# Optimization experiments

Hardware: AMD Instinct MI355X
Metric: run time of the kernel (lower is better)

## Reference

```python
import jax, jax.numpy as jnp
import numpy as np


def _lstm(x, w_ih, w_hh, b_ih, b_hh):
    """Single-layer LSTM over x: [T, in_dim], PyTorch gate order (i, f, g, o).
    Returns (all hidden states [T, H], final hidden [H])."""
    H = w_hh.shape[1]
    # Precompute input contributions for all timesteps in one GEMM: [T, 4H]
    xg = x @ w_ih.T + b_ih + b_hh

    def step(carry, xg_t):
        h, c = carry
        g = xg_t + h @ w_hh.T  # [4H]
        i = jax.nn.sigmoid(g[:H])
        f = jax.nn.sigmoid(g[H:2 * H])
        gg = jnp.tanh(g[2 * H:3 * H])
        o = jax.nn.sigmoid(g[3 * H:])
        c = f * c + i * gg
        h = o * jnp.tanh(c)
        return (h, c), h

    init = (jnp.zeros((H,), x.dtype), jnp.zeros((H,), x.dtype))
    (h_n, _), hs = jax.lax.scan(step, init, xg)
    return hs, h_n


def setup_inputs() -> dict:
    key = jax.random.key(0)
    ks = jax.random.split(key, 9)
    T, F, E = 8192, 256, 512
    Hd = 2 * E  # hidden_dim of rnn1 = 1024
    s = 0.05
    return {
        "x": jax.random.normal(ks[0], (T, F), jnp.float32),
        "w_ih1": jax.random.normal(ks[1], (4 * Hd, F), jnp.float32) * s,
        "w_hh1": jax.random.normal(ks[2], (4 * Hd, Hd), jnp.float32) * s,
        "b_ih1": jax.random.normal(ks[3], (4 * Hd,), jnp.float32) * s,
        "b_hh1": jax.random.normal(ks[4], (4 * Hd,), jnp.float32) * s,
        "w_ih2": jax.random.normal(ks[5], (4 * E, Hd), jnp.float32) * s,
        "w_hh2": jax.random.normal(ks[6], (4 * E, E), jnp.float32) * s,
        "b_ih2": jax.random.normal(ks[7], (4 * E,), jnp.float32) * s,
        "b_hh2": jax.random.normal(ks[8], (4 * E,), jnp.float32) * s,
    }


def reference(x, w_ih1, w_hh1, b_ih1, b_hh1, w_ih2, w_hh2, b_ih2, b_hh2):
    # x reshaped to (1, seq_len, n_features) in torch; batch=1 so work on [T, F].
    hs1, _ = _lstm(x, w_ih1, w_hh1, b_ih1, b_hh1)        # [T, hidden_dim]
    _, h_n = _lstm(hs1, w_ih2, w_hh2, b_ih2, b_hh2)      # [encoding_dim]
    return h_n.reshape((1, -1))                          # (1, encoding_dim)
```

## Files before the change

### kernel.cpp

```cpp
#include <hip/hip_runtime.h>
#include <cstdint>

#define TSTEPS 8192
#define FIN 256
#define HD 1024
#define ED 512
#define W1 128
#define W2 64

#define AG __HIP_MEMORY_SCOPE_AGENT
typedef unsigned long long u64;
typedef unsigned int u32;
typedef u32 u32x4 __attribute__((ext_vector_type(4)));
typedef u32 u32x2 __attribute__((ext_vector_type(2)));

#define DONE1_OFS 12288
#define DONE2_OFS 12416
#define CONS2_OFS 12480

__global__ void init_ctrs(u32* ws32) {
  int i = threadIdx.x;
  if (i < 256) ws32[DONE1_OFS + i] = 0xFFFFFFFFu;
}

__device__ __forceinline__ float sigf(float z) { return 1.0f / (1.0f + expf(-z)); }
__device__ __forceinline__ float uaf(u32 v) { return __uint_as_float(v); }

#define BULK16(pb, want, OK, q0,q1,q2,q3,q4,q5,q6,q7)                          \
  asm volatile(                                                                \
    "global_load_dwordx4 %0, %8, off sc0 sc1\n\t"                              \
    "global_load_dwordx4 %1, %8, off offset:16 sc0 sc1\n\t"                    \
    "global_load_dwordx4 %2, %8, off offset:32 sc0 sc1\n\t"                    \
    "global_load_dwordx4 %3, %8, off offset:48 sc0 sc1\n\t"                    \
    "global_load_dwordx4 %4, %8, off offset:64 sc0 sc1\n\t"                    \
    "global_load_dwordx4 %5, %8, off offset:80 sc0 sc1\n\t"                    \
    "global_load_dwordx4 %6, %8, off offset:96 sc0 sc1\n\t"                    \
    "global_load_dwordx4 %7, %8, off offset:112 sc0 sc1\n\t"                   \
    "s_waitcnt vmcnt(0)"                                                       \
    : "=&v"(q0), "=&v"(q1), "=&v"(q2), "=&v"(q3),                              \
      "=&v"(q4), "=&v"(q5), "=&v"(q6), "=&v"(q7)                               \
    : "v"(pb) : "memory");                                                     \
  OK = (q0.x==want)&(q0.z==want)&(q1.x==want)&(q1.z==want)                     \
     & (q2.x==want)&(q2.z==want)&(q3.x==want)&(q3.z==want)                     \
     & (q4.x==want)&(q4.z==want)&(q5.x==want)&(q5.z==want)                     \
     & (q6.x==want)&(q6.z==want)&(q7.x==want)&(q7.z==want);

__global__ void __launch_bounds__(256, 1) lstm2_fused(
    const float* __restrict__ x,
    const float* __restrict__ w_ih1, const float* __restrict__ w_hh1,
    const float* __restrict__ b_ih1, const float* __restrict__ b_hh1,
    const float* __restrict__ w_ih2, const float* __restrict__ w_hh2,
    const float* __restrict__ b_ih2, const float* __restrict__ b_hh2,
    float* __restrict__ out, u32* __restrict__ ws32)
{
  u64* pair1 = (u64*)ws32;
  u64* pair2 = pair1 + 4 * HD;
  u32* done1 = ws32 + DONE1_OFS;
  u32* done2 = ws32 + DONE2_OFS;
  u32* cons2 = ws32 + CONS2_OFS;

  const int bid  = blockIdx.x;
  const int tid  = threadIdx.x;
  const int wave = tid >> 6;
  const int lane = tid & 63;
  const int half = lane & 1;
  const int kc   = lane >> 1;

  __shared__ float4 hsl[256];
  __shared__ float4 h2l[128];

  if (bid < W1) {
    const int ro = bid * 8 + wave * 2 + half;
    const int kbase  = kc * 32;
    const int xkbase = kc * 8;
    float whh[4][32], wih[4][8], bz[4];
#pragma unroll
    for (int g = 0; g < 4; ++g) {
      const float* wr = w_hh1 + ((size_t)(g * HD + ro)) * HD + kbase;
#pragma unroll
      for (int j = 0; j < 8; ++j) {
        float4 v = *(const float4*)(wr + j * 4);
        whh[g][j*4+0] = v.x; whh[g][j*4+1] = v.y; whh[g][j*4+2] = v.z; whh[g][j*4+3] = v.w;
      }
      const float* ur = w_ih1 + ((size_t)(g * HD + ro)) * FIN + xkbase;
      float4 a = *(const float4*)(ur), b = *(const float4*)(ur + 4);
      wih[g][0]=a.x; wih[g][1]=a.y; wih[g][2]=a.z; wih[g][3]=a.w;
      wih[g][4]=b.x; wih[g][5]=b.y; wih[g][6]=b.z; wih[g][7]=b.w;
      bz[g] = b_ih1[g * HD + ro] + b_hh1[g * HD + ro];
    }
    float cst = 0.f;

    for (int t = 0; t < TSTEPS; ++t) {
      const float* xp = x + (size_t)t * FIN + xkbase;
      float4 xa = *(const float4*)(xp);
      float4 xb = *(const float4*)(xp + 4);

      if (t == 0) {
        hsl[tid] = make_float4(0.f, 0.f, 0.f, 0.f);
      } else if (wave == 0) {
        const u32* d1p = done1 + lane * 2;
        const u32* c2p = cons2 + lane;
        const int wd = t - 1, wc = t - 4;
        u32x2 dv; u32 cv;
        for (;;) {
          asm volatile(
            "global_load_dwordx2 %0, %2, off sc0 sc1\n\t"
            "global_load_dword %1, %3, off sc0 sc1\n\t"
            "s_waitcnt vmcnt(0)"
            : "=&v"(dv), "=&v"(cv) : "v"(d1p), "v"(c2p) : "memory");
          bool ok = ((int)dv.x >= wd) & ((int)dv.y >= wd) & ((int)cv >= wc);
          if (__all(ok)) break;
        }
        const u64* pb = pair1 + (size_t)((t - 1) & 3) * HD + lane * 16;
        const u32 want = (u32)(t - 1);
        u32x4 q0,q1,q2,q3,q4,q5,q6,q7; bool ok;
        for (;;) { BULK16(pb, want, ok, q0,q1,q2,q3,q4,q5,q6,q7); if (__all(ok)) break; }
        const int f0 = lane * 4;
        hsl[(f0+0) ^ (((f0+0)>>3)&7)] = make_float4(uaf(q0.y),uaf(q0.w),uaf(q1.y),uaf(q1.w));
        hsl[(f0+1) ^ (((f0+1)>>3)&7)] = make_float4(uaf(q2.y),uaf(q2.w),uaf(q3.y),uaf(q3.w));
        hsl[(f0+2) ^ (((f0+2)>>3)&7)] = make_float4(uaf(q4.y),uaf(q4.w),uaf(q5.y),uaf(q5.w));
        hsl[(f0+3) ^ (((f0+3)>>3)&7)] = make_float4(uaf(q6.y),uaf(q6.w),uaf(q7.y),uaf(q7.w));
      }
      __syncthreads();

      float hv[32];
#pragma unroll
      for (int j = 0; j < 8; ++j) {
        int f = kc * 8 + j;
        float4 v = hsl[f ^ ((f>>3)&7)];
        hv[j*4+0]=v.x; hv[j*4+1]=v.y; hv[j*4+2]=v.z; hv[j*4+3]=v.w;
      }

      float a0=0.f, a1=0.f, a2=0.f, a3=0.f;
#pragma unroll
      for (int j = 0; j < 32; ++j) {
        float hj = hv[j];
        a0 = fmaf(whh[0][j], hj, a0); a1 = fmaf(whh[1][j], hj, a1);
        a2 = fmaf(whh[2][j], hj, a2); a3 = fmaf(whh[3][j], hj, a3);
      }
      float xvv[8] = {xa.x,xa.y,xa.z,xa.w,xb.x,xb.y,xb.z,xb.w};
#pragma unroll
      for (int j = 0; j < 8; ++j) {
        float xj = xvv[j];
        a0 = fmaf(wih[0][j], xj, a0); a1 = fmaf(wih[1][j], xj, a1);
        a2 = fmaf(wih[2][j], xj, a2); a3 = fmaf(wih[3][j], xj, a3);
      }
#pragma unroll
      for (int d = 2; d < 64; d <<= 1) {
        a0 += __shfl_xor(a0, d, 64);
        a1 += __shfl_xor(a1, d, 64);
        a2 += __shfl_xor(a2, d, 64);
        a3 += __shfl_xor(a3, d, 64);
      }
      float ig = sigf(a0 + bz[0]);
      float fg = sigf(a1 + bz[1]);
      float gg = tanhf(a2 + bz[2]);
      float og = sigf(a3 + bz[3]);
      cst = fg * cst + ig * gg;
      float h = og * tanhf(cst);

      if (lane < 2) {
        u64 pk = ((u64)__float_as_uint(h) << 32) | (u64)(u32)t;
        __hip_atomic_store(pair1 + (size_t)(t & 3) * HD + ro, pk, __ATOMIC_RELAXED, AG);
      }
      __builtin_amdgcn_s_barrier();
      if (tid == 0)
        __hip_atomic_store(done1 + bid, (u32)t, __ATOMIC_RELAXED, AG);
    }
  } else {
    const int jwg = bid - W1;
    const int eo = jwg * 8 + wave * 2 + half;
    const int kbase  = kc * 32;
    const int k2base = kc * 16;
    float wA[4][32], wB[4][16], bz[4];
#pragma unroll
    for (int g = 0; g < 4; ++g) {
      const float* wr = w_ih2 + ((size_t)(g * ED + eo)) * HD + kbase;
#pragma unroll
      for (int j = 0; j < 8; ++j) {
        float4 v = *(const float4*)(wr + j * 4);
        wA[g][j*4+0]=v.x; wA[g][j*4+1]=v.y; wA[g][j*4+2]=v.z; wA[g][j*4+3]=v.w;
      }
      const float* wr2 = w_hh2 + ((size_t)(g * ED + eo)) * ED + k2base;
#pragma unroll
      for (int j = 0; j < 4; ++j) {
        float4 v = *(const float4*)(wr2 + j * 4);
        wB[g][j*4+0]=v.x; wB[g][j*4+1]=v.y; wB[g][j*4+2]=v.z; wB[g][j*4+3]=v.w;
      }
      bz[g] = b_ih2[g * ED + eo] + b_hh2[g * ED + eo];
    }
    float cst = 0.f;

    for (int s = 0; s < TSTEPS; ++s) {
      if (wave == 0) {
        const u32* d1p = done1 + lane * 2;
        u32x2 dv;
        for (;;) {
          asm volatile(
            "global_load_dwordx2 %0, %1, off sc0 sc1\n\t"
            "s_waitcnt vmcnt(0)"
            : "=&v"(dv) : "v"(d1p) : "memory");
          bool ok = ((int)dv.x >= s) & ((int)dv.y >= s);
          if (__all(ok)) break;
        }
        const u64* pb = pair1 + (size_t)(s & 3) * HD + lane * 16;
        const u32 want = (u32)s;
        u32x4 q0,q1,q2,q3,q4,q5,q6,q7; bool ok;
        for (;;) { BULK16(pb, want, ok, q0,q1,q2,q3,q4,q5,q6,q7); if (__all(ok)) break; }
        if (lane == 0)
          __hip_atomic_store(cons2 + jwg, (u32)s, __ATOMIC_RELAXED, AG);
        const int f0 = lane * 4;
        hsl[(f0+0) ^ (((f0+0)>>3)&7)] = make_float4(uaf(q0.y),uaf(q0.w),uaf(q1.y),uaf(q1.w));
        hsl[(f0+1) ^ (((f0+1)>>3)&7)] = make_float4(uaf(q2.y),uaf(q2.w),uaf(q3.y),uaf(q3.w));
        hsl[(f0+2) ^ (((f0+2)>>3)&7)] = make_float4(uaf(q4.y),uaf(q4.w),uaf(q5.y),uaf(q5.w));
        hsl[(f0+3) ^ (((f0+3)>>3)&7)] = make_float4(uaf(q6.y),uaf(q6.w),uaf(q7.y),uaf(q7.w));
      } else if (wave == 1 && s >= 1) {
        const u32* d2p = done2 + lane;
        const int wd = s - 1;
        u32 dv;
        for (;;) {
          asm volatile(
            "global_load_dword %0, %1, off sc0 sc1\n\t"
            "s_waitcnt vmcnt(0)"
            : "=&v"(dv) : "v"(d2p) : "memory");
          if (__all((int)dv >= wd)) break;
        }
        const u64* pb2 = pair2 + (size_t)((s - 1) & 3) * ED + lane * 8;
        const u32 want = (u32)(s - 1);
        u32x4 q0,q1,q2,q3; bool ok;
        for (;;) {
          asm volatile(
            "global_load_dwordx4 %0, %4, off sc0 sc1\n\t"
            "global_load_dwordx4 %1, %4, off offset:16 sc0 sc1\n\t"
            "global_load_dwordx4 %2, %4, off offset:32 sc0 sc1\n\t"
            "global_load_dwordx4 %3, %4, off offset:48 sc0 sc1\n\t"
            "s_waitcnt vmcnt(0)"
            : "=&v"(q0), "=&v"(q1), "=&v"(q2), "=&v"(q3)
            : "v"(pb2) : "memory");
          ok = (q0.x==want)&(q0.z==want)&(q1.x==want)&(q1.z==want)
             & (q2.x==want)&(q2.z==want)&(q3.x==want)&(q3.z==want);
          if (__all(ok)) break;
        }
        const int f0 = lane * 2;
        h2l[(f0+0) ^ (((f0+0)>>3)&7)] = make_float4(uaf(q0.y),uaf(q0.w),uaf(q1.y),uaf(q1.w));
        h2l[(f0+1) ^ (((f0+1)>>3)&7)] = make_float4(uaf(q2.y),uaf(q2.w),uaf(q3.y),uaf(q3.w));
      }
      if (s == 0 && tid < 128) h2l[tid] = make_float4(0.f, 0.f, 0.f, 0.f);
      __syncthreads();

      float hv[32];
#pragma unroll
      for (int j = 0; j < 8; ++j) {
        int f = kc * 8 + j;
        float4 v = hsl[f ^ ((f>>3)&7)];
        hv[j*4+0]=v.x; hv[j*4+1]=v.y; hv[j*4+2]=v.z; hv[j*4+3]=v.w;
      }
      float gv[16];
#pragma unroll
      for (int j = 0; j < 4; ++j) {
        int f = kc * 4 + j;
        float4 v = h2l[f ^ ((f>>3)&7)];
        gv[j*4+0]=v.x; gv[j*4+1]=v.y; gv[j*4+2]=v.z; gv[j*4+3]=v.w;
      }

      float a0=0.f, a1=0.f, a2=0.f, a3=0.f;
#pragma unroll
      for (int j = 0; j < 32; ++j) {
        float hj = hv[j];
        a0 = fmaf(wA[0][j], hj, a0); a1 = fmaf(wA[1][j], hj, a1);
        a2 = fmaf(wA[2][j], hj, a2); a3 = fmaf(wA[3][j], hj, a3);
      }
#pragma unroll
      for (int j = 0; j < 16; ++j) {
        float gj = gv[j];
        a0 = fmaf(wB[0][j], gj, a0); a1 = fmaf(wB[1][j], gj, a1);
        a2 = fmaf(wB[2][j], gj, a2); a3 = fmaf(wB[3][j], gj, a3);
      }
#pragma unroll
      for (int d = 2; d < 64; d <<= 1) {
        a0 += __shfl_xor(a0, d, 64);
        a1 += __shfl_xor(a1, d, 64);
        a2 += __shfl_xor(a2, d, 64);
        a3 += __shfl_xor(a3, d, 64);
      }
      float ig = sigf(a0 + bz[0]);
      float fg = sigf(a1 + bz[1]);
      float gg = tanhf(a2 + bz[2]);
      float og = sigf(a3 + bz[3]);
      cst = fg * cst + ig * gg;
      float h = og * tanhf(cst);

      if (lane < 2) {
        u64 pk = ((u64)__float_as_uint(h) << 32) | (u64)(u32)s;
        __hip_atomic_store(pair2 + (size_t)(s & 3) * ED + eo, pk, __ATOMIC_RELAXED, AG);
        if (s == TSTEPS - 1) out[eo] = h;
      }
      __builtin_amdgcn_s_barrier();
      if (tid == 0)
        __hip_atomic_store(done2 + jwg, (u32)s, __ATOMIC_RELAXED, AG);
    }
  }
}

extern "C" void kernel_launch(void* const* d_in, const int* in_sizes, int n_in,
                              void* d_out, int out_size, void* d_ws, size_t ws_size,
                              hipStream_t stream) {
  const float* x    = (const float*)d_in[0];
  const float* wih1 = (const float*)d_in[1];
  const float* whh1 = (const float*)d_in[2];
  const float* bih1 = (const float*)d_in[3];
  const float* bhh1 = (const float*)d_in[4];
  const float* wih2 = (const float*)d_in[5];
  const float* whh2 = (const float*)d_in[6];
  const float* bih2 = (const float*)d_in[7];
  const float* bhh2 = (const float*)d_in[8];
  float* out = (float*)d_out;
  u32* ws    = (u32*)d_ws;

  hipLaunchKernelGGL(init_ctrs, dim3(1), dim3(256), 0, stream, ws);
  hipLaunchKernelGGL(lstm2_fused, dim3(W1 + W2), dim3(256), 0, stream,
                     x, wih1, whh1, bih1, bhh1, wih2, whh2, bih2, bhh2, out, ws);
}
```

Measured before the change: 36.21 ms.

## Add per-XCC relay blocks that mirror hidden states into XCC-local buffers

Adds extra relay workgroups. One per XCC claims the role via CAS, then polls the global hidden-state ring and copies each step into an XCC-local copy. Compute blocks then poll that local copy with sc0-only loads instead of system-coherent ones, so the cross-XCC coherence traffic of the polling is paid once per XCC rather than per block. The change also removes the done-counter barriers in favour of tag-only checks, deepens the ring to 8 slots, double-buffers LDS and restructures the FMA loops. It relies on relay blocks landing on every XCC and on plain stores becoming visible to sc0 loads. A stale-count fallback to the global buffer guards against a missing relay.

```diff
diff --git a/kernel.cpp b/kernel.cpp
--- a/kernel.cpp
+++ b/kernel.cpp
@@ -7,45 +7,65 @@
 #define ED 512
 #define W1 128
 #define W2 64
-
+#define NREL 16
 #define AG __HIP_MEMORY_SCOPE_AGENT
+#define STALE_MAX 8192
+
 typedef unsigned long long u64;
 typedef unsigned int u32;
 typedef u32 u32x4 __attribute__((ext_vector_type(4)));
-typedef u32 u32x2 __attribute__((ext_vector_type(2)));
-
-#define DONE1_OFS 12288
-#define DONE2_OFS 12416
-#define CONS2_OFS 12480
+
+#define CONS2_U32  24576
+#define CLAIM1_U32 24640
+#define CLAIM2_U32 24648
+#define LOCAL_BYTE 131072
+#define XSTRIDE    131072
+#define LP2_BYTE   65536
+#define LMIN_BYTE  98304
 
 __global__ void init_ctrs(u32* ws32) {
   int i = threadIdx.x;
-  if (i < 256) ws32[DONE1_OFS + i] = 0xFFFFFFFFu;
+  if (i < 80) ws32[CONS2_U32 + i] = 0xFFFFFFFFu;
+  if (i >= 80 && i < 88)
+    *(u32*)((char*)ws32 + LOCAL_BYTE + (size_t)(i - 80) * XSTRIDE + LMIN_BYTE) = 0xFFFFFFFFu;
 }
 
 __device__ __forceinline__ float sigf(float z) { return 1.0f / (1.0f + expf(-z)); }
 __device__ __forceinline__ float uaf(u32 v) { return __uint_as_float(v); }
 
-#define BULK16(pb, want, OK, q0,q1,q2,q3,q4,q5,q6,q7)                          \
+#define TAGOK8(want,q0,q1,q2,q3,q4,q5,q6,q7)                                   \
+  ((q0.x==want)&(q0.z==want)&(q1.x==want)&(q1.z==want)&                        \
+   (q2.x==want)&(q2.z==want)&(q3.x==want)&(q3.z==want)&                        \
+   (q4.x==want)&(q4.z==want)&(q5.x==want)&(q5.z==want)&                        \
+   (q6.x==want)&(q6.z==want)&(q7.x==want)&(q7.z==want))
+
+#define LOAD8P(F, pb, cp, q0,q1,q2,q3,q4,q5,q6,q7, cv)                         \
   asm volatile(                                                                \
-    "global_load_dwordx4 %0, %8, off sc0 sc1\n\t"                              \
-    "global_load_dwordx4 %1, %8, off offset:16 sc0 sc1\n\t"                    \
-    "global_load_dwordx4 %2, %8, off offset:32 sc0 sc1\n\t"                    \
-    "global_load_dwordx4 %3, %8, off offset:48 sc0 sc1\n\t"                    \
-    "global_load_dwordx4 %4, %8, off offset:64 sc0 sc1\n\t"                    \
-    "global_load_dwordx4 %5, %8, off offset:80 sc0 sc1\n\t"                    \
-    "global_load_dwordx4 %6, %8, off offset:96 sc0 sc1\n\t"                    \
-    "global_load_dwordx4 %7, %8, off offset:112 sc0 sc1\n\t"                   \
+    "global_load_dwordx4 %0, %9, off " F "\n\t"                                \
+    "global_load_dwordx4 %1, %9, off offset:16 " F "\n\t"                      \
+    "global_load_dwordx4 %2, %9, off offset:32 " F "\n\t"                      \
+    "global_load_dwordx4 %3, %9, off offset:48 " F "\n\t"                      \
+    "global_load_dwordx4 %4, %9, off offset:64 " F "\n\t"                      \
+    "global_load_dwordx4 %5, %9, off offset:80 " F "\n\t"                      \
+    "global_load_dwordx4 %6, %9, off offset:96 " F "\n\t"                      \
+    "global_load_dwordx4 %7, %9, off offset:112 " F "\n\t"                     \
+    "global_load_dword %8, %10, off " F "\n\t"                                 \
     "s_waitcnt vmcnt(0)"                                                       \
-    : "=&v"(q0), "=&v"(q1), "=&v"(q2), "=&v"(q3),                              \
-      "=&v"(q4), "=&v"(q5), "=&v"(q6), "=&v"(q7)                               \
-    : "v"(pb) : "memory");                                                     \
-  OK = (q0.x==want)&(q0.z==want)&(q1.x==want)&(q1.z==want)                     \
-     & (q2.x==want)&(q2.z==want)&(q3.x==want)&(q3.z==want)                     \
-     & (q4.x==want)&(q4.z==want)&(q5.x==want)&(q5.z==want)                     \
-     & (q6.x==want)&(q6.z==want)&(q7.x==want)&(q7.z==want);
-
-__global__ void __launch_bounds__(256, 1) lstm2_fused(
+    : "=&v"(q0),"=&v"(q1),"=&v"(q2),"=&v"(q3),                                 \
+      "=&v"(q4),"=&v"(q5),"=&v"(q6),"=&v"(q7),"=&v"(cv)                        \
+    : "v"(pb), "v"(cp) : "memory")
+
+#define LOAD4P(F, pb, q0,q1,q2,q3)                                             \
+  asm volatile(                                                                \
+    "global_load_dwordx4 %0, %4, off " F "\n\t"                                \
+    "global_load_dwordx4 %1, %4, off offset:16 " F "\n\t"                      \
+    "global_load_dwordx4 %2, %4, off offset:32 " F "\n\t"                      \
+    "global_load_dwordx4 %3, %4, off offset:48 " F "\n\t"                      \
+    "s_waitcnt vmcnt(0)"                                                       \
+    : "=&v"(q0),"=&v"(q1),"=&v"(q2),"=&v"(q3)                                  \
+    : "v"(pb) : "memory")
+
+__global__ void __launch_bounds__(256, 2) lstm2_fused(
     const float* __restrict__ x,
     const float* __restrict__ w_ih1, const float* __restrict__ w_hh1,
     const float* __restrict__ b_ih1, const float* __restrict__ b_hh1,
@@ -53,26 +73,98 @@
     const float* __restrict__ b_ih2, const float* __restrict__ b_hh2,
     float* __restrict__ out, u32* __restrict__ ws32)
 {
-  u64* pair1 = (u64*)ws32;
-  u64* pair2 = pair1 + 4 * HD;
-  u32* done1 = ws32 + DONE1_OFS;
-  u32* done2 = ws32 + DONE2_OFS;
-  u32* cons2 = ws32 + CONS2_OFS;
+  u64* mp1 = (u64*)ws32;
+  u64* mp2 = mp1 + 8 * HD;
+  u32* cons2 = ws32 + CONS2_U32;
 
   const int bid  = blockIdx.x;
   const int tid  = threadIdx.x;
   const int wave = tid >> 6;
   const int lane = tid & 63;
-  const int half = lane & 1;
-  const int kc   = lane >> 1;
-
-  __shared__ float4 hsl[256];
-  __shared__ float4 h2l[128];
+
+  int xcc;
+  asm volatile("s_getreg_b32 %0, hwreg(HW_REG_XCC_ID)" : "=s"(xcc));
+  xcc &= 7;
+  char* lbase = (char*)ws32 + LOCAL_BYTE + (size_t)xcc * XSTRIDE;
+  u64* lp1  = (u64*)lbase;
+  u64* lp2  = (u64*)(lbase + LP2_BYTE);
+  u32* lmin = (u32*)(lbase + LMIN_BYTE);
+
+  __shared__ float4 hsl[2 * 256];
+  __shared__ float4 h2l[2 * 128];
+  __shared__ int sClaim;
+
+  if (bid >= W1 + W2) {
+    const int kind = (bid - W1 - W2) < NREL ? 0 : 1;
+    if (tid == 0) {
+      u32 exp = 0xFFFFFFFFu;
+      bool win = __hip_atomic_compare_exchange_strong(
+          ws32 + (kind ? CLAIM2_U32 : CLAIM1_U32) + xcc, &exp, (u32)bid,
+          __ATOMIC_RELAXED, __ATOMIC_RELAXED, AG);
+      sClaim = win ? 1 : 0;
+    }
+    __syncthreads();
+    if (!sClaim) return;
+
+    if (kind == 0) {
+      const int base = wave * 256 + lane * 4;
+      for (int t = 0; t < TSTEPS; ++t) {
+        const u64* src = mp1 + (size_t)(t & 7) * HD + base;
+        u64* dst = lp1 + (size_t)(t & 7) * HD + base;
+        const u32 want = (u32)t;
+        u32x4 a, b;
+        for (;;) {
+          asm volatile(
+            "global_load_dwordx4 %0, %2, off sc0 sc1\n\t"
+            "global_load_dwordx4 %1, %2, off offset:16 sc0 sc1\n\t"
+            "s_waitcnt vmcnt(0)"
+            : "=&v"(a), "=&v"(b) : "v"(src) : "memory");
+          bool ok = (a.x==want)&(a.z==want)&(b.x==want)&(b.z==want);
+          if (__all(ok)) break;
+        }
+        *(u32x4*)dst = a;
+        *(u32x4*)(dst + 2) = b;
+      }
+    } else {
+      const int base = wave * 128 + lane * 2;
+      const u32* c2p = cons2 + lane;
+      for (int s = 0; s < TSTEPS; ++s) {
+        const u64* src = mp2 + (size_t)(s & 7) * ED + base;
+        u64* dst = lp2 + (size_t)(s & 7) * ED + base;
+        const u32 want = (u32)s;
+        u32x4 a;
+        for (;;) {
+          if (wave == 0) {
+            u32 cw;
+            asm volatile(
+              "global_load_dwordx4 %0, %2, off sc0 sc1\n\t"
+              "global_load_dword %1, %3, off sc0 sc1\n\t"
+              "s_waitcnt vmcnt(0)"
+              : "=&v"(a), "=&v"(cw) : "v"(src), "v"(c2p) : "memory");
+            int m = (int)cw;
+#pragma unroll
+            for (int d = 1; d < 64; d <<= 1) m = min(m, __shfl_xor(m, d, 64));
+            if (lane == 0) *lmin = (u32)m;
+          } else {
+            asm volatile(
+              "global_load_dwordx4 %0, %1, off sc0 sc1\n\t"
+              "s_waitcnt vmcnt(0)"
+              : "=&v"(a) : "v"(src) : "memory");
+          }
+          bool ok = (a.x==want)&(a.z==want);
+          if (__all(ok)) break;
+        }
+        *(u32x4*)dst = a;
+      }
+    }
+    return;
+  }
 
   if (bid < W1) {
-    const int ro = bid * 8 + wave * 2 + half;
-    const int kbase  = kc * 32;
-    const int xkbase = kc * 8;
+    const int half = lane & 1;
+    const int kc   = lane >> 1;
+    const int ro   = bid * 8 + wave * 2 + half;
+    const int kbase = kc * 32, xkbase = kc * 8;
     float whh[4][32], wih[4][8], bz[4];
 #pragma unroll
     for (int g = 0; g < 4; ++g) {
@@ -80,7 +172,7 @@
 #pragma unroll
       for (int j = 0; j < 8; ++j) {
         float4 v = *(const float4*)(wr + j * 4);
-        whh[g][j*4+0] = v.x; whh[g][j*4+1] = v.y; whh[g][j*4+2] = v.z; whh[g][j*4+3] = v.w;
+        whh[g][j*4+0]=v.x; whh[g][j*4+1]=v.y; whh[g][j*4+2]=v.z; whh[g][j*4+3]=v.w;
       }
       const float* ur = w_ih1 + ((size_t)(g * HD + ro)) * FIN + xkbase;
       float4 a = *(const float4*)(ur), b = *(const float4*)(ur + 4);
@@ -89,61 +181,65 @@
       bz[g] = b_ih1[g * HD + ro] + b_hh1[g * HD + ro];
     }
     float cst = 0.f;
+    bool useM = false;
 
     for (int t = 0; t < TSTEPS; ++t) {
       const float* xp = x + (size_t)t * FIN + xkbase;
       float4 xa = *(const float4*)(xp);
       float4 xb = *(const float4*)(xp + 4);
+      const int sb = (t & 1) * 256;
 
       if (t == 0) {
         hsl[tid] = make_float4(0.f, 0.f, 0.f, 0.f);
       } else if (wave == 0) {
-        const u32* d1p = done1 + lane * 2;
-        const u32* c2p = cons2 + lane;
-        const int wd = t - 1, wc = t - 4;
-        u32x2 dv; u32 cv;
+        const int slot = (t - 1) & 7;
+        const u32 want = (u32)(t - 1);
+        const int bp = t - 8;
+        const u64* lpb = lp1 + (size_t)slot * HD + lane * 16;
+        const u64* mpb = mp1 + (size_t)slot * HD + lane * 16;
+        const u32* mcp = cons2 + lane;
+        u32x4 q0,q1,q2,q3,q4,q5,q6,q7; u32 cv;
+        int stale = 0;
         for (;;) {
-          asm volatile(
-            "global_load_dwordx2 %0, %2, off sc0 sc1\n\t"
-            "global_load_dword %1, %3, off sc0 sc1\n\t"
-            "s_waitcnt vmcnt(0)"
-            : "=&v"(dv), "=&v"(cv) : "v"(d1p), "v"(c2p) : "memory");
-          bool ok = ((int)dv.x >= wd) & ((int)dv.y >= wd) & ((int)cv >= wc);
-          if (__all(ok)) break;
+          if (!useM) {
+            LOAD8P("sc0", lpb, lmin, q0,q1,q2,q3,q4,q5,q6,q7, cv);
+            bool ok = TAGOK8(want,q0,q1,q2,q3,q4,q5,q6,q7) & ((int)cv >= bp);
+            if (__all(ok)) break;
+            if (++stale > STALE_MAX) useM = true;
+          } else {
+            LOAD8P("sc0 sc1", mpb, mcp, q0,q1,q2,q3,q4,q5,q6,q7, cv);
+            bool ok = TAGOK8(want,q0,q1,q2,q3,q4,q5,q6,q7) & ((int)cv >= bp);
+            if (__all(ok)) break;
+          }
         }
-        const u64* pb = pair1 + (size_t)((t - 1) & 3) * HD + lane * 16;
-        const u32 want = (u32)(t - 1);
-        u32x4 q0,q1,q2,q3,q4,q5,q6,q7; bool ok;
-        for (;;) { BULK16(pb, want, ok, q0,q1,q2,q3,q4,q5,q6,q7); if (__all(ok)) break; }
         const int f0 = lane * 4;
-        hsl[(f0+0) ^ (((f0+0)>>3)&7)] = make_float4(uaf(q0.y),uaf(q0.w),uaf(q1.y),uaf(q1.w));
-        hsl[(f0+1) ^ (((f0+1)>>3)&7)] = make_float4(uaf(q2.y),uaf(q2.w),uaf(q3.y),uaf(q3.w));
-        hsl[(f0+2) ^ (((f0+2)>>3)&7)] = make_float4(uaf(q4.y),uaf(q4.w),uaf(q5.y),uaf(q5.w));
-        hsl[(f0+3) ^ (((f0+3)>>3)&7)] = make_float4(uaf(q6.y),uaf(q6.w),uaf(q7.y),uaf(q7.w));
+        hsl[sb + ((f0+0) ^ (((f0+0)>>3)&7))] = make_float4(uaf(q0.y),uaf(q0.w),uaf(q1.y),uaf(q1.w));
+        hsl[sb + ((f0+1) ^ (((f0+1)>>3)&7))] = make_float4(uaf(q2.y),uaf(q2.w),uaf(q3.y),uaf(q3.w));
+        hsl[sb + ((f0+2) ^ (((f0+2)>>3)&7))] = make_float4(uaf(q4.y),uaf(q4.w),uaf(q5.y),uaf(q5.w));
+        hsl[sb + ((f0+3) ^ (((f0+3)>>3)&7))] = make_float4(uaf(q6.y),uaf(q6.w),uaf(q7.y),uaf(q7.w));
       }
       __syncthreads();
 
-      float hv[32];
+      float a0=0.f, a1=0.f, a2=0.f, a3=0.f;
 #pragma unroll
       for (int j = 0; j < 8; ++j) {
-        int f = kc * 8 + j;
-        float4 v = hsl[f ^ ((f>>3)&7)];
-        hv[j*4+0]=v.x; hv[j*4+1]=v.y; hv[j*4+2]=v.z; hv[j*4+3]=v.w;
-      }
-
-      float a0=0.f, a1=0.f, a2=0.f, a3=0.f;
-#pragma unroll
-      for (int j = 0; j < 32; ++j) {
-        float hj = hv[j];
-        a0 = fmaf(whh[0][j], hj, a0); a1 = fmaf(whh[1][j], hj, a1);
-        a2 = fmaf(whh[2][j], hj, a2); a3 = fmaf(whh[3][j], hj, a3);
+        const int f = kc * 8 + (j ^ (kc & 7));
+        float4 v = hsl[sb + f];
+        a0=fmaf(whh[0][j*4+0],v.x,a0); a0=fmaf(whh[0][j*4+1],v.y,a0);
+        a0=fmaf(whh[0][j*4+2],v.z,a0); a0=fmaf(whh[0][j*4+3],v.w,a0);
+        a1=fmaf(whh[1][j*4+0],v.x,a1); a1=fmaf(whh[1][j*4+1],v.y,a1);
+        a1=fmaf(whh[1][j*4+2],v.z,a1); a1=fmaf(whh[1][j*4+3],v.w,a1);
+        a2=fmaf(whh[2][j*4+0],v.x,a2); a2=fmaf(whh[2][j*4+1],v.y,a2);
+        a2=fmaf(whh[2][j*4+2],v.z,a2); a2=fmaf(whh[2][j*4+3],v.w,a2);
+        a3=fmaf(whh[3][j*4+0],v.x,a3); a3=fmaf(whh[3][j*4+1],v.y,a3);
+        a3=fmaf(whh[3][j*4+2],v.z,a3); a3=fmaf(whh[3][j*4+3],v.w,a3);
       }
       float xvv[8] = {xa.x,xa.y,xa.z,xa.w,xb.x,xb.y,xb.z,xb.w};
 #pragma unroll
       for (int j = 0; j < 8; ++j) {
         float xj = xvv[j];
-        a0 = fmaf(wih[0][j], xj, a0); a1 = fmaf(wih[1][j], xj, a1);
-        a2 = fmaf(wih[2][j], xj, a2); a3 = fmaf(wih[3][j], xj, a3);
+        a0=fmaf(wih[0][j],xj,a0); a1=fmaf(wih[1][j],xj,a1);
+        a2=fmaf(wih[2][j],xj,a2); a3=fmaf(wih[3][j],xj,a3);
       }
 #pragma unroll
       for (int d = 2; d < 64; d <<= 1) {
@@ -161,17 +257,15 @@
 
       if (lane < 2) {
         u64 pk = ((u64)__float_as_uint(h) << 32) | (u64)(u32)t;
-        __hip_atomic_store(pair1 + (size_t)(t & 3) * HD + ro, pk, __ATOMIC_RELAXED, AG);
-      }
-      __builtin_amdgcn_s_barrier();
-      if (tid == 0)
-        __hip_atomic_store(done1 + bid, (u32)t, __ATOMIC_RELAXED, AG);
+        __hip_atomic_store(mp1 + (size_t)(t & 7) * HD + ro, pk, __ATOMIC_RELAXED, AG);
+      }
     }
   } else {
-    const int jwg = bid - W1;
-    const int eo = jwg * 8 + wave * 2 + half;
-    const int kbase  = kc * 32;
-    const int k2base = kc * 16;
+    const int jwg  = bid - W1;
+    const int half = lane & 1;
+    const int kc   = lane >> 1;
+    const int eo   = jwg * 8 + wave * 2 + half;
+    const int kbase = kc * 32, k2base = kc * 16;
     float wA[4][32], wB[4][16], bz[4];
 #pragma unroll
     for (int g = 0; g < 4; ++g) {
@@ -190,91 +284,95 @@
       bz[g] = b_ih2[g * ED + eo] + b_hh2[g * ED + eo];
     }
     float cst = 0.f;
+    bool useM0 = false, useM1 = false;
 
     for (int s = 0; s < TSTEPS; ++s) {
+      const int sb  = (s & 1) * 256;
+      const int sb2 = (s & 1) * 128;
+
       if (wave == 0) {
-        const u32* d1p = done1 + lane * 2;
-        u32x2 dv;
+        const int slot = s & 7;
+        const u32 want = (u32)s;
+        const u64* lpb = lp1 + (size_t)slot * HD + lane * 16;
+        const u64* mpb = mp1 + (size_t)slot * HD + lane * 16;
+        u32x4 q0,q1,q2,q3,q4,q5,q6,q7; u32 cv;
+        int stale = 0;
         for (;;) {
-          asm volatile(
-            "global_load_dwordx2 %0, %1, off sc0 sc1\n\t"
-            "s_waitcnt vmcnt(0)"
-            : "=&v"(dv) : "v"(d1p) : "memory");
-          bool ok = ((int)dv.x >= s) & ((int)dv.y >= s);
-          if (__all(ok)) break;
+          if (!useM0) {
+            LOAD8P("sc0", lpb, lmin, q0,q1,q2,q3,q4,q5,q6,q7, cv);
+            if (__all(TAGOK8(want,q0,q1,q2,q3,q4,q5,q6,q7))) break;
+            if (++stale > STALE_MAX) useM0 = true;
+          } else {
+            LOAD8P("sc0 sc1", mpb, lmin, q0,q1,q2,q3,q4,q5,q6,q7, cv);
+            if (__all(TAGOK8(want,q0,q1,q2,q3,q4,q5,q6,q7))) break;
+          }
         }
-        const u64* pb = pair1 + (size_t)(s & 3) * HD + lane * 16;
-        const u32 want = (u32)s;
-        u32x4 q0,q1,q2,q3,q4,q5,q6,q7; bool ok;
-        for (;;) { BULK16(pb, want, ok, q0,q1,q2,q3,q4,q5,q6,q7); if (__all(ok)) break; }
         if (lane == 0)
           __hip_atomic_store(cons2 + jwg, (u32)s, __ATOMIC_RELAXED, AG);
         const int f0 = lane * 4;
-        hsl[(f0+0) ^ (((f0+0)>>3)&7)] = make_float4(uaf(q0.y),uaf(q0.w),uaf(q1.y),uaf(q1.w));
-        hsl[(f0+1) ^ (((f0+1)>>3)&7)] = make_float4(uaf(q2.y),uaf(q2.w),uaf(q3.y),uaf(q3.w));
-        hsl[(f0+2) ^ (((f0+2)>>3)&7)] = make_float4(uaf(q4.y),uaf(q4.w),uaf(q5.y),uaf(q5.w));
-        hsl[(f0+3) ^ (((f0+3)>>3)&7)] = make_float4(uaf(q6.y),uaf(q6.w),uaf(q7.y),uaf(q7.w));
-      } else if (wave == 1 && s >= 1) {
-        const u32* d2p = done2 + lane;
-        const int wd = s - 1;
-        u32 dv;
-        for (;;) {
-          asm volatile(
-            "global_load_dword %0, %1, off sc0 sc1\n\t"
-            "s_waitcnt vmcnt(0)"
-            : "=&v"(dv) : "v"(d2p) : "memory");
-          if (__all((int)dv >= wd)) break;
+        hsl[sb + ((f0+0) ^ (((f0+0)>>3)&7))] = make_float4(uaf(q0.y),uaf(q0.w),uaf(q1.y),uaf(q1.w));
+        hsl[sb + ((f0+1) ^ (((f0+1)>>3)&7))] = make_float4(uaf(q2.y),uaf(q2.w),uaf(q3.y),uaf(q3.w));
+        hsl[sb + ((f0+2) ^ (((f0+2)>>3)&7))] = make_float4(uaf(q4.y),uaf(q4.w),uaf(q5.y),uaf(q5.w));
+        hsl[sb + ((f0+3) ^ (((f0+3)>>3)&7))] = make_float4(uaf(q6.y),uaf(q6.w),uaf(q7.y),uaf(q7.w));
+      } else if (wave == 1) {
+        if (s == 0) {
+          h2l[lane * 2] = make_float4(0.f,0.f,0.f,0.f);
+          h2l[lane * 2 + 1] = make_float4(0.f,0.f,0.f,0.f);
+        } else {
+          const int slot = (s - 1) & 7;
+          const u32 want = (u32)(s - 1);
+          const u64* lpb = lp2 + (size_t)slot * ED + lane * 8;
+          const u64* mpb = mp2 + (size_t)slot * ED + lane * 8;
+          u32x4 q0,q1,q2,q3;
+          int stale = 0;
+          for (;;) {
+            if (!useM1) {
+              LOAD4P("sc0", lpb, q0,q1,q2,q3);
+              bool ok = (q0.x==want)&(q0.z==want)&(q1.x==want)&(q1.z==want)
+                      & (q2.x==want)&(q2.z==want)&(q3.x==want)&(q3.z==want);
+              if (__all(ok)) break;
+              if (++stale > STALE_MAX) useM1 = true;
+            } else {
+              LOAD4P("sc0 sc1", mpb, q0,q1,q2,q3);
+              bool ok = (q0.x==want)&(q0.z==want)&(q1.x==want)&(q1.z==want)
+                      & (q2.x==want)&(q2.z==want)&(q3.x==want)&(q3.z==want);
+              if (__all(ok)) break;
+            }
+          }
+          const int f0 = lane * 2;
+          h2l[sb2 + ((f0+0) ^ (((f0+0)>>3)&7))] = make_float4(uaf(q0.y),uaf(q0.w),uaf(q1.y),uaf(q1.w));
+          h2l[sb2 + ((f0+1) ^ (((f0+1)>>3)&7))] = make_float4(uaf(q2.y),uaf(q2.w),uaf(q3.y),uaf(q3.w));
         }
-        const u64* pb2 = pair2 + (size_t)((s - 1) & 3) * ED + lane * 8;
-        const u32 want = (u32)(s - 1);
-        u32x4 q0,q1,q2,q3; bool ok;
-        for (;;) {
-          asm volatile(
-            "global_load_dwordx4 %0, %4, off sc0 sc1\n\t"
-            "global_load_dwordx4 %1, %4, off offset:16 sc0 sc1\n\t"
-            "global_load_dwordx4 %2, %4, off offset:32 sc0 sc1\n\t"
-            "global_load_dwordx4 %3, %4, off offset:48 sc0 sc1\n\t"
-            "s_waitcnt vmcnt(0)"
-            : "=&v"(q0), "=&v"(q1), "=&v"(q2), "=&v"(q3)
-            : "v"(pb2) : "memory");
-          ok = (q0.x==want)&(q0.z==want)&(q1.x==want)&(q1.z==want)
-             & (q2.x==want)&(q2.z==want)&(q3.x==want)&(q3.z==want);
-          if (__all(ok)) break;
-        }
-        const int f0 = lane * 2;
-        h2l[(f0+0) ^ (((f0+0)>>3)&7)] = make_float4(uaf(q0.y),uaf(q0.w),uaf(q1.y),uaf(q1.w));
-        h2l[(f0+1) ^ (((f0+1)>>3)&7)] = make_float4(uaf(q2.y),uaf(q2.w),uaf(q3.y),uaf(q3.w));
-      }
-      if (s == 0 && tid < 128) h2l[tid] = make_float4(0.f, 0.f, 0.f, 0.f);
+      }
       __syncthreads();
 
-      float hv[32];
+      float a0=0.f, a1=0.f, a2=0.f, a3=0.f;
 #pragma unroll
       for (int j = 0; j < 8; ++j) {
-        int f = kc * 8 + j;
-        float4 v = hsl[f ^ ((f>>3)&7)];
-        hv[j*4+0]=v.x; hv[j*4+1]=v.y; hv[j*4+2]=v.z; hv[j*4+3]=v.w;
-      }
-      float gv[16];
+        const int f = kc * 8 + (j ^ (kc & 7));
+        float4 v = hsl[sb + f];
+        a0=fmaf(wA[0][j*4+0],v.x,a0); a0=fmaf(wA[0][j*4+1],v.y,a0);
+        a0=fmaf(wA[0][j*4+2],v.z,a0); a0=fmaf(wA[0][j*4+3],v.w,a0);
+        a1=fmaf(wA[1][j*4+0],v.x,a1); a1=fmaf(wA[1][j*4+1],v.y,a1);
+        a1=fmaf(wA[1][j*4+2],v.z,a1); a1=fmaf(wA[1][j*4+3],v.w,a1);
+        a2=fmaf(wA[2][j*4+0],v.x,a2); a2=fmaf(wA[2][j*4+1],v.y,a2);
+        a2=fmaf(wA[2][j*4+2],v.z,a2); a2=fmaf(wA[2][j*4+3],v.w,a2);
+        a3=fmaf(wA[3][j*4+0],v.x,a3); a3=fmaf(wA[3][j*4+1],v.y,a3);
+        a3=fmaf(wA[3][j*4+2],v.z,a3); a3=fmaf(wA[3][j*4+3],v.w,a3);
+      }
 #pragma unroll
       for (int j = 0; j < 4; ++j) {
-        int f = kc * 4 + j;
-        float4 v = h2l[f ^ ((f>>3)&7)];
-        gv[j*4+0]=v.x; gv[j*4+1]=v.y; gv[j*4+2]=v.z; gv[j*4+3]=v.w;
-      }
-
-      float a0=0.f, a1=0.f, a2=0.f, a3=0.f;
-#pragma unroll
-      for (int j = 0; j < 32; ++j) {
-        float hj = hv[j];
-        a0 = fmaf(wA[0][j], hj, a0); a1 = fmaf(wA[1][j], hj, a1);
-        a2 = fmaf(wA[2][j], hj, a2); a3 = fmaf(wA[3][j], hj, a3);
-      }
-#pragma unroll
-      for (int j = 0; j < 16; ++j) {
-        float gj = gv[j];
-        a0 = fmaf(wB[0][j], gj, a0); a1 = fmaf(wB[1][j], gj, a1);
-        a2 = fmaf(wB[2][j], gj, a2); a3 = fmaf(wB[3][j], gj, a3);
+        int L = kc * 4 + j;
+        const int f = L ^ ((L >> 3) & 7);
+        float4 v = h2l[sb2 + f];
+        a0=fmaf(wB[0][j*4+0],v.x,a0); a0=fmaf(wB[0][j*4+1],v.y,a0);
+        a0=fmaf(wB[0][j*4+2],v.z,a0); a0=fmaf(wB[0][j*4+3],v.w,a0);
+        a1=fmaf(wB[1][j*4+0],v.x,a1); a1=fmaf(wB[1][j*4+1],v.y,a1);
+        a1=fmaf(wB[1][j*4+2],v.z,a1); a1=fmaf(wB[1][j*4+3],v.w,a1);
+        a2=fmaf(wB[2][j*4+0],v.x,a2); a2=fmaf(wB[2][j*4+1],v.y,a2);
+        a2=fmaf(wB[2][j*4+2],v.z,a2); a2=fmaf(wB[2][j*4+3],v.w,a2);
+        a3=fmaf(wB[3][j*4+0],v.x,a3); a3=fmaf(wB[3][j*4+1],v.y,a3);
+        a3=fmaf(wB[3][j*4+2],v.z,a3); a3=fmaf(wB[3][j*4+3],v.w,a3);
       }
 #pragma unroll
       for (int d = 2; d < 64; d <<= 1) {
@@ -292,12 +390,9 @@
 
       if (lane < 2) {
         u64 pk = ((u64)__float_as_uint(h) << 32) | (u64)(u32)s;
-        __hip_atomic_store(pair2 + (size_t)(s & 3) * ED + eo, pk, __ATOMIC_RELAXED, AG);
+        __hip_atomic_store(mp2 + (size_t)(s & 7) * ED + eo, pk, __ATOMIC_RELAXED, AG);
         if (s == TSTEPS - 1) out[eo] = h;
       }
-      __builtin_amdgcn_s_barrier();
-      if (tid == 0)
-        __hip_atomic_store(done2 + jwg, (u32)s, __ATOMIC_RELAXED, AG);
     }
   }
 }
@@ -317,7 +412,7 @@
   float* out = (float*)d_out;
   u32* ws    = (u32*)d_ws;
 
-  hipLaunchKernelGGL(init_ctrs, dim3(1), dim3(256), 0, stream, ws);
-  hipLaunchKernelGGL(lstm2_fused, dim3(W1 + W2), dim3(256), 0, stream,
+  hipLaunchKernelGGL(init_ctrs, dim3(1), dim3(128), 0, stream, ws);
+  hipLaunchKernelGGL(lstm2_fused, dim3(W1 + W2 + 2 * NREL), dim3(256), 0, stream,
                      x, wih1, whh1, bih1, bhh1, wih2, whh2, bih2, bhh2, out, ws);
 }
```

Result: slower. 56.53 ms (+56.1%).
